# Kernel tuning notes

Measured on AMD Instinct MI355X. Metric: run time of the kernel, lower is better.

Reference implementation:

```python
import jax, jax.numpy as jnp
import numpy as np

T, B, D, H = 512, 32, 1024, 1024


def setup_inputs() -> dict:
    key = jax.random.key(0)
    k1, k2, k3, k4, k5 = jax.random.split(key, 5)
    s = 1.0 / np.sqrt(H)
    return {
        "input": jax.random.normal(k1, (T, B, D), dtype=jnp.float32),
        "paddings": jnp.zeros((T, B, 1), dtype=jnp.float32),
        "W_ih": jax.random.uniform(k2, (D, 3 * H), jnp.float32, -s, s),
        "W_hh": jax.random.uniform(k3, (H, 3 * H), jnp.float32, -s, s),
        "b_ih": jax.random.uniform(k4, (3 * H,), jnp.float32, -s, s),
        "b_hh": jax.random.uniform(k5, (3 * H,), jnp.float32, -s, s),
    }


def reference(input, paddings, W_ih, W_hh, b_ih, b_hh):
    # GRU cell per step with padding carry-through (padding==1 -> keep prev state).
    def step(h, xp):
        x, p = xp  # x: [B, D], p: [B, 1]
        gi = x @ W_ih + b_ih          # [B, 3H]
        gh = h @ W_hh + b_hh          # [B, 3H]
        i_r, i_z, i_n = jnp.split(gi, 3, axis=-1)
        h_r, h_z, h_n = jnp.split(gh, 3, axis=-1)
        r = jax.nn.sigmoid(i_r + h_r)
        z = jax.nn.sigmoid(i_z + h_z)
        n = jnp.tanh(i_n + r * h_n)
        h_new = (1.0 - z) * n + z * h
        h_new = p * h + (1.0 - p) * h_new
        return h_new, h_new

    h0 = jnp.zeros((input.shape[1], H), dtype=input.dtype)
    h_last, outputs = jax.lax.scan(step, h0, (input, paddings))
    # matches torch module: (stacked outputs, (last output, final state))
    return outputs, (outputs[-1], h_last)
```

## Files before the change

### kernel.cpp

```cpp
#include <hip/hip_runtime.h>
#include <cmath>


typedef short s8v  __attribute__((ext_vector_type(8)));
typedef float f4v  __attribute__((ext_vector_type(4)));

#define NB 64
#define GUARD 16384

__device__ __forceinline__ short f2bf(float f) {
    return __builtin_bit_cast(short, (__bf16)f);
}
__device__ __forceinline__ float bf2f(short s) {
    return (float)__builtin_bit_cast(__bf16, s);
}

__global__ __launch_bounds__(256) void k_transpose_bf16(
        const float* __restrict__ W, short* __restrict__ Wt) {
    __shared__ short Ls[32][72];
    int bk = blockIdx.x & 31;
    int bn = blockIdx.x >> 5;
    int k0 = bk * 32, n0 = bn * 64;
    int tid = threadIdx.x;
    {
        int r  = tid >> 3;
        int c0 = (tid & 7) * 8;
        const float* src = W + (size_t)(k0 + r) * 3072 + n0 + c0;
        float4 f0 = *reinterpret_cast<const float4*>(src);
        float4 f1 = *reinterpret_cast<const float4*>(src + 4);
        Ls[r][c0+0] = f2bf(f0.x); Ls[r][c0+1] = f2bf(f0.y);
        Ls[r][c0+2] = f2bf(f0.z); Ls[r][c0+3] = f2bf(f0.w);
        Ls[r][c0+4] = f2bf(f1.x); Ls[r][c0+5] = f2bf(f1.y);
        Ls[r][c0+6] = f2bf(f1.z); Ls[r][c0+7] = f2bf(f1.w);
    }
    __syncthreads();
    {
        int j   = tid >> 2;
        int kk0 = (tid & 3) * 8;
        s8v v;
        #pragma unroll
        for (int s = 0; s < 8; ++s) v[s] = Ls[kk0 + s][j];
        *reinterpret_cast<s8v*>(Wt + (size_t)(n0 + j) * 1024 + k0 + kk0) = v;
    }
}

__global__ __launch_bounds__(256) void k_gemm_gi(
        const float* __restrict__ X, const short* __restrict__ Wt,
        short* __restrict__ gi) {
    __shared__ short As[64][40];
    __shared__ short Bs[64][40];
    int bm = blockIdx.x & 255;
    int bn = blockIdx.x >> 8;
    int m0 = bm * 64, n0 = bn * 64;
    int tid = threadIdx.x;
    int wid = tid >> 6, l = tid & 63;
    int wm = wid >> 1, wn = wid & 1;
    int lr = l & 15, q = l >> 4;
    f4v acc[2][2] = {};
    int sr = tid >> 2;
    int sc = (tid & 3) * 8;

    for (int kc = 0; kc < 1024; kc += 32) {
        const float* asrc = X + (size_t)(m0 + sr) * 1024 + kc + sc;
        float4 f0 = *reinterpret_cast<const float4*>(asrc);
        float4 f1 = *reinterpret_cast<const float4*>(asrc + 4);
        s8v av;
        av[0]=f2bf(f0.x); av[1]=f2bf(f0.y); av[2]=f2bf(f0.z); av[3]=f2bf(f0.w);
        av[4]=f2bf(f1.x); av[5]=f2bf(f1.y); av[6]=f2bf(f1.z); av[7]=f2bf(f1.w);
        *reinterpret_cast<s8v*>(&As[sr][sc]) = av;
        *reinterpret_cast<s8v*>(&Bs[sr][sc]) =
            *reinterpret_cast<const s8v*>(Wt + (size_t)(n0 + sr) * 1024 + kc + sc);
        __syncthreads();
        s8v a0 = *reinterpret_cast<const s8v*>(&As[wm*32 +  0 + lr][q*8]);
        s8v a1 = *reinterpret_cast<const s8v*>(&As[wm*32 + 16 + lr][q*8]);
        s8v b0 = *reinterpret_cast<const s8v*>(&Bs[wn*32 +  0 + lr][q*8]);
        s8v b1 = *reinterpret_cast<const s8v*>(&Bs[wn*32 + 16 + lr][q*8]);
        acc[0][0] = __builtin_amdgcn_mfma_f32_16x16x32_bf16(a0, b0, acc[0][0], 0,0,0);
        acc[0][1] = __builtin_amdgcn_mfma_f32_16x16x32_bf16(a0, b1, acc[0][1], 0,0,0);
        acc[1][0] = __builtin_amdgcn_mfma_f32_16x16x32_bf16(a1, b0, acc[1][0], 0,0,0);
        acc[1][1] = __builtin_amdgcn_mfma_f32_16x16x32_bf16(a1, b1, acc[1][1], 0,0,0);
        __syncthreads();
    }
    #pragma unroll
    for (int ms = 0; ms < 2; ++ms)
      #pragma unroll
      for (int ns = 0; ns < 2; ++ns) {
        int m = m0 + wm*32 + ms*16 + q*4;
        int n = n0 + wn*32 + ns*16 + lr;
        #pragma unroll
        for (int i = 0; i < 4; ++i)
            gi[(size_t)(m + i) * 3072 + n] = f2bf(acc[ms][ns][i]);
      }
}

__global__ __launch_bounds__(128, 1) void k_gru(
        const float* __restrict__ pad,
        const short* __restrict__ gi,
        const short* __restrict__ Whht,
        const float* __restrict__ b_ih,
        const float* __restrict__ b_hh,
        unsigned long long* __restrict__ hb4,
        unsigned* __restrict__ flags,
        float* __restrict__ out) {
    extern __shared__ short wlds[];
    const int WS = 1032;
    int bid = blockIdx.x;
    int j0  = bid * 16;
    int tid = threadIdx.x;
    int w   = tid >> 6;
    int l   = tid & 63, lr = l & 15, q = l >> 4;

    for (int idx = tid; idx < 48 * 128; idx += 128) {
        int row = idx >> 7;
        int ko  = (idx & 127) * 8;
        int g = row >> 4, c = row & 15;
        *reinterpret_cast<s8v*>(&wlds[(g * 16 + c) * WS + ko]) =
            *reinterpret_cast<const s8v*>(Whht + (size_t)(g * 1024 + j0 + c) * 1024 + ko);
    }
    __syncthreads();

    int jq = j0 + q * 4;
    int b  = w * 16 + lr;
    f4v sbr = *reinterpret_cast<const f4v*>(b_ih + jq)
            + *reinterpret_cast<const f4v*>(b_hh + jq);
    f4v sbz = *reinterpret_cast<const f4v*>(b_ih + 1024 + jq)
            + *reinterpret_cast<const f4v*>(b_hh + 1024 + jq);
    f4v sbn_i = *reinterpret_cast<const f4v*>(b_ih + 2048 + jq);
    f4v sbn_h = *reinterpret_cast<const f4v*>(b_hh + 2048 + jq);
    const short* w_r = &wlds[(0 * 16 + lr) * WS + q * 8];
    const short* w_z = &wlds[(1 * 16 + lr) * WS + q * 8];
    const short* w_n = &wlds[(2 * 16 + lr) * WS + q * 8];
    float hp[4] = {0.f, 0.f, 0.f, 0.f};

    const unsigned* myflag = flags + w * 64 + l;

    int m_  = bid * 4 + q;
    int kk_ = ((m_ >> 3) << 1) | (m_ & 1);
    int sl_ = ((m_ & 7) >> 1) * 16 + lr;
    unsigned long long* hw0 = hb4 + (size_t)w * 4096 + kk_ * 64 + sl_;
    unsigned long long* hw1 = hw0 + 8192;
    const unsigned long long* hc0 = hb4 + (size_t)w * 4096 + l;
    const unsigned long long* hc1 = hc0 + 8192;

    union u64s { unsigned long long u; short s[4]; };
    u64s gr_, gz_, gn_; float pv;
    {
        const short* gp = gi + (size_t)b * 3072 + jq;
        gr_.u = *reinterpret_cast<const unsigned long long*>(gp);
        gz_.u = *reinterpret_cast<const unsigned long long*>(gp + 1024);
        gn_.u = *reinterpret_cast<const unsigned long long*>(gp + 2048);
        pv = pad[b];
    }

    for (int t = 0; t < 512; ++t) {
        if (t) {
            unsigned uT = (unsigned)t;
            int g1 = 0;
            for (;;) {
                unsigned f = __hip_atomic_load(myflag, __ATOMIC_RELAXED,
                                               __HIP_MEMORY_SCOPE_AGENT);
                if (__all((int)(f >= uT))) break;
                if (++g1 > GUARD) break;
                __builtin_amdgcn_s_sleep(1);
            }
        }

        const unsigned long long* hbase = (t & 1) ? hc1 : hc0;
        unsigned long long hreg[64];
        #pragma unroll
        for (int k = 0; k < 64; ++k)
            hreg[k] = __hip_atomic_load(hbase + (size_t)k * 64,
                                        __ATOMIC_RELAXED, __HIP_MEMORY_SCOPE_AGENT);

        f4v ar = {0,0,0,0}, az = {0,0,0,0}, an = {0,0,0,0};
        #pragma unroll
        for (int it = 0; it < 32; ++it) {
            union { unsigned long long u[2]; s8v v; } hx;
            hx.u[0] = hreg[2*it]; hx.u[1] = hreg[2*it+1];
            s8v r8 = *reinterpret_cast<const s8v*>(w_r + it * 32);
            s8v z8 = *reinterpret_cast<const s8v*>(w_z + it * 32);
            s8v n8 = *reinterpret_cast<const s8v*>(w_n + it * 32);
            ar = __builtin_amdgcn_mfma_f32_16x16x32_bf16(r8, hx.v, ar, 0,0,0);
            az = __builtin_amdgcn_mfma_f32_16x16x32_bf16(z8, hx.v, az, 0,0,0);
            an = __builtin_amdgcn_mfma_f32_16x16x32_bf16(n8, hx.v, an, 0,0,0);
        }

        #pragma unroll
        for (int i = 0; i < 4; ++i) {
            float xr = bf2f(gr_.s[i]) + ar[i] + sbr[i];
            float xz = bf2f(gz_.s[i]) + az[i] + sbz[i];
            float r  = __builtin_amdgcn_rcpf(1.f + __expf(-xr));
            float z  = __builtin_amdgcn_rcpf(1.f + __expf(-xz));
            float xn = bf2f(gn_.s[i]) + sbn_i[i] + r * (an[i] + sbn_h[i]);
            float e2 = __expf(2.f * xn);
            float n  = 1.f - 2.f * __builtin_amdgcn_rcpf(1.f + e2);
            float hnv = (1.f - z) * n + z * hp[i];
            hnv = pv * hp[i] + (1.f - pv) * hnv;
            hp[i] = hnv;
        }

        int rowg = t * 32 + b;

        if (t < 511) {
            u64s pk;
            pk.s[0] = f2bf(hp[0]); pk.s[1] = f2bf(hp[1]);
            pk.s[2] = f2bf(hp[2]); pk.s[3] = f2bf(hp[3]);
            unsigned long long* hwr = ((t + 1) & 1) ? hw1 : hw0;
            __hip_atomic_store(hwr, pk.u, __ATOMIC_RELAXED, __HIP_MEMORY_SCOPE_AGENT);
            __builtin_amdgcn_s_waitcnt(0);
            if (l == 0)
                __hip_atomic_store(flags + w * 64 + bid, (unsigned)(t + 1),
                                   __ATOMIC_RELAXED, __HIP_MEMORY_SCOPE_AGENT);
        }

        float4 o4 = { hp[0], hp[1], hp[2], hp[3] };
        *reinterpret_cast<float4*>(out + (size_t)rowg * 1024 + jq) = o4;
        if (t == 511) {
            *reinterpret_cast<float4*>(out + 16777216 + b * 1024 + jq) = o4;
            *reinterpret_cast<float4*>(out + 16809984 + b * 1024 + jq) = o4;
        }

        if (t < 511) {
            const short* gp = gi + (size_t)((t + 1) * 32 + b) * 3072 + jq;
            gr_.u = *reinterpret_cast<const unsigned long long*>(gp);
            gz_.u = *reinterpret_cast<const unsigned long long*>(gp + 1024);
            gn_.u = *reinterpret_cast<const unsigned long long*>(gp + 2048);
            pv = pad[(t + 1) * 32 + b];
        }
    }
}

extern "C" void kernel_launch(void* const* d_in, const int* in_sizes, int n_in,
                              void* d_out, int out_size, void* d_ws, size_t ws_size,
                              hipStream_t stream) {
    const float* X   = (const float*)d_in[0];
    const float* pad = (const float*)d_in[1];
    const float* Wih = (const float*)d_in[2];
    const float* Whh = (const float*)d_in[3];
    const float* bih = (const float*)d_in[4];
    const float* bhh = (const float*)d_in[5];
    float* out = (float*)d_out;

    char* ws = (char*)d_ws;
    short*    gi    = (short*)(ws);
    short*    Wih_t = (short*)(ws + 100663296);
    short*    Whh_t = (short*)(ws + 106954752);
    unsigned long long* hb4 =
        (unsigned long long*)(ws + 100663296);
    unsigned* flags = (unsigned*)(ws + 100663296 + 131072);

    hipLaunchKernelGGL(k_transpose_bf16, dim3(1536), dim3(256), 0, stream, Wih, Wih_t);
    hipLaunchKernelGGL(k_transpose_bf16, dim3(1536), dim3(256), 0, stream, Whh, Whh_t);
    hipLaunchKernelGGL(k_gemm_gi, dim3(256 * 48), dim3(256), 0, stream, X, Wih_t, gi);

    hipMemsetAsync(hb4, 0, 131072 + 512, stream);

    hipFuncSetAttribute((const void*)k_gru,
                        hipFuncAttributeMaxDynamicSharedMemorySize, 99072);
    hipLaunchKernelGGL(k_gru, dim3(NB), dim3(128), 99072, stream,
                       pad, gi, Whh_t, bih, bhh, hb4, flags, out);
}
```

Measured before the change: 2.562 ms.

## Enlarge input-projection GEMM tiles and pipeline per-chunk flag waits in GRU recurrence

The input-projection GEMM tile grows from 64x64 to 128x128 with a 4x4 MFMA accumulator grid per wave, raising data reuse per LDS load and cutting the block count. The recurrent kernel no longer waits for every producer flag before loading the hidden state. It takes a ballot of flags and waits only on the producers owning each 32-wide chunk, and it software-pipelines the hidden-state loads four chunks ahead of the MFMAs. This lets compute on early chunks overlap with late-arriving producers, at the cost of more register pressure and repeated ballots.

Result: slower. 2.809 ms (+9.6%).

```diff
diff --git a/kernel.cpp b/kernel.cpp
--- a/kernel.cpp
+++ b/kernel.cpp
@@ -47,46 +47,57 @@
 __global__ __launch_bounds__(256) void k_gemm_gi(
         const float* __restrict__ X, const short* __restrict__ Wt,
         short* __restrict__ gi) {
-    __shared__ short As[64][40];
-    __shared__ short Bs[64][40];
-    int bm = blockIdx.x & 255;
-    int bn = blockIdx.x >> 8;
-    int m0 = bm * 64, n0 = bn * 64;
+    __shared__ short As[128][40];
+    __shared__ short Bs[128][40];
+    int bm = blockIdx.x & 127;
+    int bn = blockIdx.x >> 7;
+    int m0 = bm * 128, n0 = bn * 128;
     int tid = threadIdx.x;
     int wid = tid >> 6, l = tid & 63;
     int wm = wid >> 1, wn = wid & 1;
     int lr = l & 15, q = l >> 4;
-    f4v acc[2][2] = {};
-    int sr = tid >> 2;
-    int sc = (tid & 3) * 8;
+    f4v acc[4][4] = {};
+    int sr = tid >> 1;
+    int sc = (tid & 1) * 16;
 
     for (int kc = 0; kc < 1024; kc += 32) {
         const float* asrc = X + (size_t)(m0 + sr) * 1024 + kc + sc;
         float4 f0 = *reinterpret_cast<const float4*>(asrc);
         float4 f1 = *reinterpret_cast<const float4*>(asrc + 4);
-        s8v av;
-        av[0]=f2bf(f0.x); av[1]=f2bf(f0.y); av[2]=f2bf(f0.z); av[3]=f2bf(f0.w);
-        av[4]=f2bf(f1.x); av[5]=f2bf(f1.y); av[6]=f2bf(f1.z); av[7]=f2bf(f1.w);
-        *reinterpret_cast<s8v*>(&As[sr][sc]) = av;
-        *reinterpret_cast<s8v*>(&Bs[sr][sc]) =
-            *reinterpret_cast<const s8v*>(Wt + (size_t)(n0 + sr) * 1024 + kc + sc);
+        float4 f2 = *reinterpret_cast<const float4*>(asrc + 8);
+        float4 f3 = *reinterpret_cast<const float4*>(asrc + 12);
+        s8v av0, av1;
+        av0[0]=f2bf(f0.x); av0[1]=f2bf(f0.y); av0[2]=f2bf(f0.z); av0[3]=f2bf(f0.w);
+        av0[4]=f2bf(f1.x); av0[5]=f2bf(f1.y); av0[6]=f2bf(f1.z); av0[7]=f2bf(f1.w);
+        av1[0]=f2bf(f2.x); av1[1]=f2bf(f2.y); av1[2]=f2bf(f2.z); av1[3]=f2bf(f2.w);
+        av1[4]=f2bf(f3.x); av1[5]=f2bf(f3.y); av1[6]=f2bf(f3.z); av1[7]=f2bf(f3.w);
+        *reinterpret_cast<s8v*>(&As[sr][sc])     = av0;
+        *reinterpret_cast<s8v*>(&As[sr][sc + 8]) = av1;
+        const short* bsrc = Wt + (size_t)(n0 + sr) * 1024 + kc + sc;
+        *reinterpret_cast<s8v*>(&Bs[sr][sc])     = *reinterpret_cast<const s8v*>(bsrc);
+        *reinterpret_cast<s8v*>(&Bs[sr][sc + 8]) = *reinterpret_cast<const s8v*>(bsrc + 8);
         __syncthreads();
-        s8v a0 = *reinterpret_cast<const s8v*>(&As[wm*32 +  0 + lr][q*8]);
-        s8v a1 = *reinterpret_cast<const s8v*>(&As[wm*32 + 16 + lr][q*8]);
-        s8v b0 = *reinterpret_cast<const s8v*>(&Bs[wn*32 +  0 + lr][q*8]);
-        s8v b1 = *reinterpret_cast<const s8v*>(&Bs[wn*32 + 16 + lr][q*8]);
-        acc[0][0] = __builtin_amdgcn_mfma_f32_16x16x32_bf16(a0, b0, acc[0][0], 0,0,0);
-        acc[0][1] = __builtin_amdgcn_mfma_f32_16x16x32_bf16(a0, b1, acc[0][1], 0,0,0);
-        acc[1][0] = __builtin_amdgcn_mfma_f32_16x16x32_bf16(a1, b0, acc[1][0], 0,0,0);
-        acc[1][1] = __builtin_amdgcn_mfma_f32_16x16x32_bf16(a1, b1, acc[1][1], 0,0,0);
+        s8v af[4], bf[4];
+        #pragma unroll
+        for (int ms = 0; ms < 4; ++ms)
+            af[ms] = *reinterpret_cast<const s8v*>(&As[wm*64 + ms*16 + lr][q*8]);
+        #pragma unroll
+        for (int ns = 0; ns < 4; ++ns)
+            bf[ns] = *reinterpret_cast<const s8v*>(&Bs[wn*64 + ns*16 + lr][q*8]);
+        #pragma unroll
+        for (int ms = 0; ms < 4; ++ms)
+            #pragma unroll
+            for (int ns = 0; ns < 4; ++ns)
+                acc[ms][ns] = __builtin_amdgcn_mfma_f32_16x16x32_bf16(
+                                  af[ms], bf[ns], acc[ms][ns], 0,0,0);
         __syncthreads();
     }
     #pragma unroll
-    for (int ms = 0; ms < 2; ++ms)
+    for (int ms = 0; ms < 4; ++ms)
       #pragma unroll
-      for (int ns = 0; ns < 2; ++ns) {
-        int m = m0 + wm*32 + ms*16 + q*4;
-        int n = n0 + wn*32 + ns*16 + lr;
+      for (int ns = 0; ns < 4; ++ns) {
+        int m = m0 + wm*64 + ms*16 + q*4;
+        int n = n0 + wn*64 + ns*16 + lr;
         #pragma unroll
         for (int i = 0; i < 4; ++i)
             gi[(size_t)(m + i) * 3072 + n] = f2bf(acc[ms][ns][i]);
@@ -153,36 +164,46 @@
     }
 
     for (int t = 0; t < 512; ++t) {
-        if (t) {
-            unsigned uT = (unsigned)t;
-            int g1 = 0;
-            for (;;) {
-                unsigned f = __hip_atomic_load(myflag, __ATOMIC_RELAXED,
-                                               __HIP_MEMORY_SCOPE_AGENT);
-                if (__all((int)(f >= uT))) break;
-                if (++g1 > GUARD) break;
-                __builtin_amdgcn_s_sleep(1);
+        unsigned uT = (unsigned)t;
+
+        unsigned long long bal;
+        {
+            unsigned f = __hip_atomic_load(myflag, __ATOMIC_RELAXED,
+                                           __HIP_MEMORY_SCOPE_AGENT);
+            bal = __ballot((int)(f >= uT));
+        }
+
+        const unsigned long long* hbase = (t & 1) ? hc1 : hc0;
+        unsigned long long ha[32], hb_[32];
+        f4v ar = {0,0,0,0}, az = {0,0,0,0}, an = {0,0,0,0};
+        #pragma unroll
+        for (int it = 0; it < 36; ++it) {
+            if (it < 32) {
+                unsigned long long need = 3ull << (2 * it);
+                int g1 = 0;
+                while ((bal & need) != need) {
+                    if (++g1 > GUARD) break;
+                    __builtin_amdgcn_s_sleep(1);
+                    unsigned f = __hip_atomic_load(myflag, __ATOMIC_RELAXED,
+                                                   __HIP_MEMORY_SCOPE_AGENT);
+                    bal = __ballot((int)(f >= uT));
+                }
+                ha[it]  = __hip_atomic_load(hbase + (2*it)     * 64,
+                              __ATOMIC_RELAXED, __HIP_MEMORY_SCOPE_AGENT);
+                hb_[it] = __hip_atomic_load(hbase + (2*it + 1) * 64,
+                              __ATOMIC_RELAXED, __HIP_MEMORY_SCOPE_AGENT);
             }
-        }
-
-        const unsigned long long* hbase = (t & 1) ? hc1 : hc0;
-        unsigned long long hreg[64];
-        #pragma unroll
-        for (int k = 0; k < 64; ++k)
-            hreg[k] = __hip_atomic_load(hbase + (size_t)k * 64,
-                                        __ATOMIC_RELAXED, __HIP_MEMORY_SCOPE_AGENT);
-
-        f4v ar = {0,0,0,0}, az = {0,0,0,0}, an = {0,0,0,0};
-        #pragma unroll
-        for (int it = 0; it < 32; ++it) {
-            union { unsigned long long u[2]; s8v v; } hx;
-            hx.u[0] = hreg[2*it]; hx.u[1] = hreg[2*it+1];
-            s8v r8 = *reinterpret_cast<const s8v*>(w_r + it * 32);
-            s8v z8 = *reinterpret_cast<const s8v*>(w_z + it * 32);
-            s8v n8 = *reinterpret_cast<const s8v*>(w_n + it * 32);
-            ar = __builtin_amdgcn_mfma_f32_16x16x32_bf16(r8, hx.v, ar, 0,0,0);
-            az = __builtin_amdgcn_mfma_f32_16x16x32_bf16(z8, hx.v, az, 0,0,0);
-            an = __builtin_amdgcn_mfma_f32_16x16x32_bf16(n8, hx.v, an, 0,0,0);
+            if (it >= 4) {
+                int jt = it - 4;
+                union { unsigned long long u[2]; s8v v; } hx;
+                hx.u[0] = ha[jt]; hx.u[1] = hb_[jt];
+                s8v r8 = *reinterpret_cast<const s8v*>(w_r + jt * 32);
+                s8v z8 = *reinterpret_cast<const s8v*>(w_z + jt * 32);
+                s8v n8 = *reinterpret_cast<const s8v*>(w_n + jt * 32);
+                ar = __builtin_amdgcn_mfma_f32_16x16x32_bf16(r8, hx.v, ar, 0,0,0);
+                az = __builtin_amdgcn_mfma_f32_16x16x32_bf16(z8, hx.v, az, 0,0,0);
+                an = __builtin_amdgcn_mfma_f32_16x16x32_bf16(n8, hx.v, an, 0,0,0);
+            }
         }
 
         #pragma unroll
@@ -251,7 +272,7 @@
 
     hipLaunchKernelGGL(k_transpose_bf16, dim3(1536), dim3(256), 0, stream, Wih, Wih_t);
     hipLaunchKernelGGL(k_transpose_bf16, dim3(1536), dim3(256), 0, stream, Whh, Whh_t);
-    hipLaunchKernelGGL(k_gemm_gi, dim3(256 * 48), dim3(256), 0, stream, X, Wih_t, gi);
+    hipLaunchKernelGGL(k_gemm_gi, dim3(128 * 24), dim3(256), 0, stream, X, Wih_t, gi);
 
     hipMemsetAsync(hb4, 0, 131072 + 512, stream);
 
```
